# Kernel tuning notes

Measured on AMD Instinct MI355X. Metric: run time of the kernel, lower is better.

The kernel has to match this reference:

```python
import jax, jax.numpy as jnp
import numpy as np

NUM_HEADS = 8
WIN = 4
DIM = 256
EPS = 1e-5


def setup_inputs() -> dict:
    key = jax.random.key(0)
    ks = jax.random.split(key, 5)
    B, C, H, W = 2, DIM, 64, 64
    features = jax.random.normal(ks[0], (B, C, H, W), dtype=jnp.float32)
    # Linear(dim, 3*dim): stored as [C, 3C] so y = x @ qkv_w + qkv_b (matches torch x @ W.T + b)
    qkv_w = jax.random.normal(ks[1], (C, 3 * C), dtype=jnp.float32) * 0.02
    qkv_b = jax.random.normal(ks[2], (3 * C,), dtype=jnp.float32) * 0.02
    out_w = jax.random.normal(ks[3], (C, C), dtype=jnp.float32) * 0.02
    out_b = jax.random.normal(ks[4], (C,), dtype=jnp.float32) * 0.02
    ln_w = jnp.ones((C,), dtype=jnp.float32)
    ln_b = jnp.zeros((C,), dtype=jnp.float32)
    return {"features": features, "qkv_w": qkv_w, "qkv_b": qkv_b,
            "out_w": out_w, "out_b": out_b, "ln_w": ln_w, "ln_b": ln_b}


def reference(features, qkv_w, qkv_b, out_w, out_b, ln_w, ln_b):
    ws = WIN
    B, C, H, W = features.shape
    hc, wc = H // ws, W // ws          # windows per col / row (H,W divisible by ws)
    nW = hc * wc
    Tq = ws * ws
    h, d = NUM_HEADS, C // NUM_HEADS

    # --- query windows: replicate torch unfold(k=ws, s=ws).transpose(1,2).reshape(.., Tq, C)
    # torch unfold layout per window is (c, ki, kj); the reshape reinterprets that flat
    # C*ws*ws vector as [ws*ws, C]. A contiguous reshape reproduces this exactly.
    qwin = features.reshape(B, C, hc, ws, wc, ws).transpose(0, 2, 4, 1, 3, 5)  # [B,hc,wc,C,ws,ws]
    q_tok = qwin.reshape(B, nW, Tq, C)
    # LayerNorm(dim) on query tokens only
    mu = q_tok.mean(-1, keepdims=True)
    var = ((q_tok - mu) ** 2).mean(-1, keepdims=True)
    q_tok = (q_tok - mu) / jnp.sqrt(var + EPS) * ln_w + ln_b

    # --- local KV: unfold(k=2*ws, s=ws) on features padded by ws//2 each side
    lk = 2 * ws
    p = ws // 2
    fp = jnp.pad(features, ((0, 0), (0, 0), (p, p), (p, p)))
    rows = jnp.arange(hc)[:, None] * ws + jnp.arange(lk)[None, :]  # [hc, lk]
    cols = jnp.arange(wc)[:, None] * ws + jnp.arange(lk)[None, :]  # [wc, lk]
    loc = fp[:, :, rows[:, None, :, None], cols[None, :, None, :]]  # [B,C,hc,wc,lk,lk]
    loc = loc.transpose(0, 2, 3, 1, 4, 5).reshape(B, nW, lk * lk, C)  # same layout replica
    Ll = lk * lk

    # --- pooled KV (computed once per batch; the torch expand is a pure broadcast)
    mid = features.reshape(B, C, H // 2, 2, W // 2, 2).mean(axis=(3, 5))
    glb = features.reshape(B, C, H // 4, 4, W // 4, 4).mean(axis=(3, 5))
    mid_tok = mid.reshape(B, C, -1).transpose(0, 2, 1)   # [B, Lm, C]
    glb_tok = glb.reshape(B, C, -1).transpose(0, 2, 1)   # [B, Lg, C]
    Lm = mid_tok.shape[1]

    # --- shared qkv projection; queries use only the Q slice, KV use only K/V slices
    q = (q_tok @ qkv_w + qkv_b)[..., :C]

    def kv(t):
        o = t @ qkv_w + qkv_b
        return o[..., C:2 * C], o[..., 2 * C:]

    kl, vl = kv(loc)
    km, vm = kv(mid_tok)
    kg, vg = kv(glb_tok)

    # heads
    q = q.reshape(B, nW, Tq, h, d).transpose(0, 1, 3, 2, 4)           # [B,nW,h,Tq,d]
    kl = kl.reshape(B, nW, Ll, h, d).transpose(0, 1, 3, 2, 4)
    vl = vl.reshape(B, nW, Ll, h, d).transpose(0, 1, 3, 2, 4)
    km = km.reshape(B, Lm, h, d).transpose(0, 2, 1, 3)                # [B,h,Lm,d]
    vm = vm.reshape(B, Lm, h, d).transpose(0, 2, 1, 3)
    kg = kg.reshape(B, -1, h, d).transpose(0, 2, 1, 3)
    vg = vg.reshape(B, -1, h, d).transpose(0, 2, 1, 3)

    scale = 1.0 / np.sqrt(d).astype(np.float32)
    s_l = jnp.einsum('bwhqd,bwhkd->bwhqk', q, kl)
    s_m = jnp.einsum('bwhqd,bhkd->bwhqk', q, km)
    s_g = jnp.einsum('bwhqd,bhkd->bwhqk', q, kg)
    attn = jax.nn.softmax(jnp.concatenate([s_l, s_m, s_g], axis=-1) * scale, axis=-1)
    a_l = attn[..., :Ll]
    a_m = attn[..., Ll:Ll + Lm]
    a_g = attn[..., Ll + Lm:]
    o = (jnp.einsum('bwhqk,bwhkd->bwhqd', a_l, vl)
         + jnp.einsum('bwhqk,bhkd->bwhqd', a_m, vm)
         + jnp.einsum('bwhqk,bhkd->bwhqd', a_g, vg))

    o = o.transpose(0, 1, 3, 2, 4).reshape(B, nW, Tq, C)
    o = o @ out_w + out_b
    # restore spatial layout: view(B,hc,wc,ws,ws,C).permute(0,5,1,3,2,4).view(B,C,H,W)
    o = o.reshape(B, hc, wc, ws, ws, C).transpose(0, 5, 1, 3, 2, 4).reshape(B, C, H, W)
    return o + features
```

## Files before the change

kernel.cpp:

```cpp
#include <hip/hip_runtime.h>
#include <math.h>

#define HWSZ 4096
#define QSCALE_L2E 0.25501988932587245f

typedef __bf16 bf16x2 __attribute__((ext_vector_type(2)));
typedef __bf16 bf16x4 __attribute__((ext_vector_type(4)));
typedef __bf16 bf16x8 __attribute__((ext_vector_type(8)));
typedef float  f32x4  __attribute__((ext_vector_type(4)));

__global__ __launch_bounds__(256) void fused_pre(
    const float* __restrict__ F, const float* __restrict__ lnw,
    const float* __restrict__ lnb, __bf16* __restrict__ qnb,
    float* __restrict__ mid, float* __restrict__ glb,
    const float* __restrict__ Wqkv, const float* __restrict__ Wout,
    __bf16* __restrict__ WT, __bf16* __restrict__ WoT)
{
  __shared__ float sbuf[64*68];
  int u = blockIdx.x;
  int tid = threadIdx.x;
  if (u < 512) {
    float* sm = sbuf;
    int blk = u;
    int b = blk >> 8, wy = (blk >> 4) & 15, t = blk & 15;
    const float* Fb = F + ((size_t)(b*256 + t*16))*HWSZ + (wy*4)*64;
    int py = tid >> 6, x = tid & 63;
    #pragma unroll
    for (int j = 0; j < 16; ++j)
      sm[j*269 + py*67 + x] = Fb[(size_t)j*HWSZ + py*64 + x];
    __syncthreads();
    int wx = tid >> 4, cl = tid & 15;
    float vals[16], s1 = 0.f, s2 = 0.f;
    #pragma unroll
    for (int p = 0; p < 16; ++p) {
      float v = sm[cl*269 + (p >> 2)*67 + wx*4 + (p & 3)];
      vals[p] = v; s1 += v; s2 += v*v;
    }
    #pragma unroll
    for (int m = 1; m < 16; m <<= 1) { s1 += __shfl_xor(s1, m); s2 += __shfl_xor(s2, m); }
    float mean = s1 * (1.f/256.f);
    float var  = s2 * (1.f/256.f) - mean*mean;
    float rstd = rsqrtf(var + 1e-5f);
    __bf16* outp = qnb + (((size_t)(b*256 + wy*16 + wx))*16 + t)*256 + cl*16;
    bf16x8 o0, o1;
    #pragma unroll
    for (int p = 0; p < 8; ++p) {
      o0[p] = (__bf16)((vals[p]  -mean)*rstd*lnw[cl*16+p]   + lnb[cl*16+p]);
      o1[p] = (__bf16)((vals[p+8]-mean)*rstd*lnw[cl*16+p+8] + lnb[cl*16+p+8]);
    }
    *(bf16x8*)outp = o0;
    *(bf16x8*)(outp+8) = o1;
  } else if (u < 1024) {
    int bc = u - 512;
    int gy = tid >> 4, gx = tid & 15;
    const float* p = F + (size_t)bc*HWSZ + (gy*4)*64 + gx*4;
    float4 r0 = *(const float4*)(p);
    float4 r1 = *(const float4*)(p + 64);
    float4 r2 = *(const float4*)(p + 128);
    float4 r3 = *(const float4*)(p + 192);
    float m00 = 0.25f*(r0.x + r0.y + r1.x + r1.y);
    float m01 = 0.25f*(r0.z + r0.w + r1.z + r1.w);
    float m10 = 0.25f*(r2.x + r2.y + r3.x + r3.y);
    float m11 = 0.25f*(r2.z + r2.w + r3.z + r3.w);
    float* mp = mid + (size_t)bc*1024 + (gy*2)*32 + gx*2;
    *(float2*)mp        = make_float2(m00, m01);
    *(float2*)(mp + 32) = make_float2(m10, m11);
    glb[(size_t)bc*256 + gy*16 + gx] = 0.25f*(m00 + m01 + m10 + m11);
  } else {
    float (*T)[68] = (float(*)[68])sbuf;
    int v = u - 1024;
    int bx = v & 15, k0 = (v >> 4)*64;
    int c4 = (tid & 15)*4, rr = tid >> 4;
    const float* W; __bf16* D; int ncols, n0;
    if (bx < 12) { W = Wqkv; D = WT;  ncols = 768; n0 = bx*64; }
    else         { W = Wout; D = WoT; ncols = 256; n0 = (bx-12)*64; }
    #pragma unroll
    for (int p = 0; p < 4; ++p) {
      int row = p*16 + rr;
      float4 vv = *(const float4*)(W + (size_t)(k0+row)*ncols + n0 + c4);
      T[c4+0][row] = vv.x; T[c4+1][row] = vv.y; T[c4+2][row] = vv.z; T[c4+3][row] = vv.w;
    }
    __syncthreads();
    #pragma unroll
    for (int p = 0; p < 4; ++p) {
      int cc = p*16 + rr;
      bf16x4 o;
      o[0] = (__bf16)T[cc][c4+0]; o[1] = (__bf16)T[cc][c4+1];
      o[2] = (__bf16)T[cc][c4+2]; o[3] = (__bf16)T[cc][c4+3];
      *(bf16x4*)(D + (size_t)(n0+cc)*256 + k0 + c4) = o;
    }
  }
}

__global__ __launch_bounds__(256) void mgt_transpose(
    const float* __restrict__ mid, const float* __restrict__ glb,
    __bf16* __restrict__ mgt)
{
  __shared__ float T[64][68];
  int tt = blockIdx.x;
  int tid = threadIdx.x;
  int c4 = (tid & 15)*4, rr = tid >> 4;
  int b = tt / 20, tq = tt % 20;
  int t0 = tq*64, c0 = blockIdx.y*64;
  const float* src; int stride, toff;
  if (t0 < 1024) { src = mid + ((size_t)(b*256 + c0))*1024; stride = 1024; toff = t0; }
  else           { src = glb + ((size_t)(b*256 + c0))*256;  stride = 256;  toff = t0 - 1024; }
  #pragma unroll
  for (int p = 0; p < 4; ++p) {
    int row = p*16 + rr;
    float4 v = *(const float4*)(src + (size_t)row*stride + toff + c4);
    T[c4+0][row] = v.x; T[c4+1][row] = v.y; T[c4+2][row] = v.z; T[c4+3][row] = v.w;
  }
  __syncthreads();
  #pragma unroll
  for (int p = 0; p < 4; ++p) {
    int t2 = p*16 + rr;
    bf16x4 o;
    o[0] = (__bf16)T[t2][c4+0]; o[1] = (__bf16)T[t2][c4+1];
    o[2] = (__bf16)T[t2][c4+2]; o[3] = (__bf16)T[t2][c4+3];
    *(bf16x4*)(mgt + ((size_t)b*1280 + t0 + t2)*256 + c0 + c4) = o;
  }
}

__global__ __launch_bounds__(256) void fused_gemms(
    const float* __restrict__ F, const __bf16* __restrict__ qnb,
    const __bf16* __restrict__ mgt, const __bf16* __restrict__ WT,
    const float* __restrict__ qkvb,
    __bf16* __restrict__ qbf, __bf16* __restrict__ kloc,
    __bf16* __restrict__ vloct, __bf16* __restrict__ kmg,
    __bf16* __restrict__ vmgt)
{
  __shared__ __bf16 Bs[2][16*264];
  int u = blockIdx.x;
  int tid = threadIdx.x;
  int wv = tid >> 6, lane = tid & 63;
  int col = lane & 15, quad = lane >> 4;
  const f32x4 zero = {0.f,0.f,0.f,0.f};

  if (u < 512) {
    int bw = u;
    int b = bw >> 8, w = bw & 255;
    int wy = w >> 4, wx = w & 15;
    int m0 = wv*16;

    bf16x8 af[8];
    int x0 = wx*4 - 2;
    bool p0ok = (wx > 0), p3ok = (wx < 15);
    const float* Fb = F + ((size_t)(b*256 + 4*(m0+col)))*HWSZ;
    #pragma unroll
    for (int kk = 0; kk < 8; ++kk) {
      int r = kk >> 1;
      int y = wy*4 + (kk & 1)*4 + quad - 2;
      bool yok = ((unsigned)y < 64u);
      const float* row = Fb + (size_t)r*HWSZ + y*64 + x0;
      float2 v0 = make_float2(0.f,0.f), v1 = make_float2(0.f,0.f);
      float2 v2 = make_float2(0.f,0.f), v3 = make_float2(0.f,0.f);
      if (yok) {
        if (p0ok) v0 = *(const float2*)(row);
        v1 = *(const float2*)(row + 2);
        v2 = *(const float2*)(row + 4);
        if (p3ok) v3 = *(const float2*)(row + 6);
      }
      af[kk][0] = (__bf16)v0.x; af[kk][1] = (__bf16)v0.y;
      af[kk][2] = (__bf16)v1.x; af[kk][3] = (__bf16)v1.y;
      af[kk][4] = (__bf16)v2.x; af[kk][5] = (__bf16)v2.y;
      af[kk][6] = (__bf16)v3.x; af[kk][7] = (__bf16)v3.y;
    }

    int brow = tid >> 4, bseg = tid & 15;
    const __bf16* wsrc = WT + ((size_t)(256 + brow))*256 + bseg*16;
    __bf16* bd0 = &Bs[0][0] + brow*264 + bseg*16;
    {
      bf16x8 a0 = *(const bf16x8*)wsrc;
      bf16x8 a1 = *(const bf16x8*)(wsrc + 8);
      *(bf16x8*)bd0 = a0;
      *(bf16x8*)(bd0 + 8) = a1;
    }
    bf16x8 g0 = *(const bf16x8*)(wsrc + (size_t)4096);
    bf16x8 g1 = *(const bf16x8*)(wsrc + (size_t)4096 + 8);
    __syncthreads();

    #pragma unroll 1
    for (int nt = 0; nt < 32; ++nt) {
      if (nt < 31) {
        __bf16* d = &Bs[(nt+1) & 1][0] + brow*264 + bseg*16;
        *(bf16x8*)d = g0;
        *(bf16x8*)(d + 8) = g1;
      }
      if (nt < 30) {
        const __bf16* p = wsrc + (size_t)(nt+2)*4096;
        g0 = *(const bf16x8*)p;
        g1 = *(const bf16x8*)(p + 8);
      }
      int n = nt*16 + col;
      float bias_n = qkvb[256 + n];
      const __bf16* Bb = &Bs[nt & 1][0] + col*264 + quad*8;
      f32x4 acc = zero;
      #pragma unroll
      for (int kk = 0; kk < 8; ++kk) {
        bf16x8 bv = *(const bf16x8*)(Bb + kk*32);
        acc = __builtin_amdgcn_mfma_f32_16x16x32_bf16(af[kk], bv, acc, 0, 0, 0);
      }
      if (nt < 16) {
        #pragma unroll
        for (int r = 0; r < 4; ++r)
          kloc[((size_t)bw*64 + m0 + quad*4 + r)*256 + n] = (__bf16)(acc[r] + bias_n);
      } else {
        bf16x4 o;
        #pragma unroll
        for (int r = 0; r < 4; ++r) o[r] = (__bf16)(acc[r] + bias_n);
        *(bf16x4*)(vloct + ((size_t)bw*256 + (n - 256))*64 + m0 + quad*4) = o;
      }
      __syncthreads();
    }
  } else if (u < 768) {
    int blk = u - 512;
    int tb = blk >> 1, nh = blk & 1;
    int n0 = nh*128;
    int m0 = tb*64 + wv*16;

    bf16x8 bq[8];
    const __bf16* qp = qnb + ((size_t)(m0 + col))*256 + quad*8;
    #pragma unroll
    for (int kk = 0; kk < 8; ++kk) bq[kk] = *(const bf16x8*)(qp + kk*32);

    int brow = tid >> 4, bseg = tid & 15;
    const __bf16* wsrc = WT + ((size_t)(n0 + brow))*256 + bseg*16;
    {
      bf16x8 a0 = *(const bf16x8*)wsrc;
      bf16x8 a1 = *(const bf16x8*)(wsrc + 8);
      __bf16* d = &Bs[0][0] + brow*264 + bseg*16;
      *(bf16x8*)d = a0; *(bf16x8*)(d + 8) = a1;
    }
    bf16x8 g0 = *(const bf16x8*)(wsrc + (size_t)4096);
    bf16x8 g1 = *(const bf16x8*)(wsrc + (size_t)4096 + 8);
    __syncthreads();

    #pragma unroll 1
    for (int s = 0; s < 8; ++s) {
      if (s < 7) {
        __bf16* d = &Bs[(s+1) & 1][0] + brow*264 + bseg*16;
        *(bf16x8*)d = g0; *(bf16x8*)(d + 8) = g1;
      }
      if (s < 6) {
        const __bf16* p = wsrc + (size_t)(s+2)*4096;
        g0 = *(const bf16x8*)p; g1 = *(const bf16x8*)(p + 8);
      }
      const __bf16* Ab = &Bs[s & 1][0] + col*264 + quad*8;
      f32x4 acc = zero;
      #pragma unroll
      for (int kk = 0; kk < 8; ++kk) {
        bf16x8 wf = *(const bf16x8*)(Ab + kk*32);
        acc = __builtin_amdgcn_mfma_f32_16x16x32_bf16(wf, bq[kk], acc, 0, 0, 0);
      }
      int nq4 = n0 + s*16 + quad*4;
      float4 b4 = *(const float4*)(qkvb + nq4);
      float bb[4] = {b4.x, b4.y, b4.z, b4.w};
      bf16x4 o;
      #pragma unroll
      for (int r = 0; r < 4; ++r) o[r] = (__bf16)((acc[r]+bb[r])*QSCALE_L2E);
      *(bf16x4*)(qbf + ((size_t)(m0 + col))*256 + nq4) = o;
      __syncthreads();
    }
  } else {
    int v = u - 768;
    int tb = v % 20, nq = (v / 20) & 3, b = v / 80;
    int m0 = tb*64 + wv*16;
    int n0 = nq*128;

    const __bf16* Ab = mgt + ((size_t)b*1280 + m0 + col)*256 + quad*8;
    bf16x8 af[8];
    #pragma unroll
    for (int kk = 0; kk < 8; ++kk) af[kk] = *(const bf16x8*)(Ab + kk*32);

    int brow = tid >> 4, bseg = tid & 15;
    const __bf16* wsrc = WT + ((size_t)(256 + n0 + brow))*256 + bseg*16;
    {
      bf16x8 a0 = *(const bf16x8*)wsrc;
      bf16x8 a1 = *(const bf16x8*)(wsrc + 8);
      __bf16* d = &Bs[0][0] + brow*264 + bseg*16;
      *(bf16x8*)d = a0; *(bf16x8*)(d + 8) = a1;
    }
    bf16x8 g0 = *(const bf16x8*)(wsrc + (size_t)4096);
    bf16x8 g1 = *(const bf16x8*)(wsrc + (size_t)4096 + 8);
    __syncthreads();

    #pragma unroll 1
    for (int s = 0; s < 8; ++s) {
      if (s < 7) {
        __bf16* d = &Bs[(s+1) & 1][0] + brow*264 + bseg*16;
        *(bf16x8*)d = g0; *(bf16x8*)(d + 8) = g1;
      }
      if (s < 6) {
        const __bf16* p = wsrc + (size_t)(s+2)*4096;
        g0 = *(const bf16x8*)p; g1 = *(const bf16x8*)(p + 8);
      }
      int n = n0 + s*16 + col;
      float bias_n = qkvb[256 + n];
      const __bf16* Bb = &Bs[s & 1][0] + col*264 + quad*8;
      f32x4 acc = zero;
      #pragma unroll
      for (int kk = 0; kk < 8; ++kk) {
        bf16x8 bv = *(const bf16x8*)(Bb + kk*32);
        acc = __builtin_amdgcn_mfma_f32_16x16x32_bf16(af[kk], bv, acc, 0, 0, 0);
      }
      if (n < 256) {
        #pragma unroll
        for (int r = 0; r < 4; ++r)
          kmg[((size_t)b*1280 + m0 + quad*4 + r)*256 + n] = (__bf16)(acc[r] + bias_n);
      } else {
        bf16x4 o;
        #pragma unroll
        for (int r = 0; r < 4; ++r) o[r] = (__bf16)(acc[r] + bias_n);
        *(bf16x4*)(vmgt + ((size_t)b*256 + (n - 256))*1280 + m0 + quad*4) = o;
      }
      __syncthreads();
    }
  }
}

__global__ __launch_bounds__(512) void attn_mfma(
    const __bf16* __restrict__ qbf, const __bf16* __restrict__ kloc,
    const __bf16* __restrict__ vloct, const __bf16* __restrict__ kmg,
    const __bf16* __restrict__ vmgt, __bf16* __restrict__ obf)
{
  __shared__ __bf16 Ks[2][64][40];
  __shared__ __bf16 Vs[2][32][72];
  __shared__ __bf16 Pb[8][2][16][40];
  int blk = blockIdx.x;
  int b = blk >> 8, rr = blk & 255;
  int h = rr >> 5, wg = rr & 31;
  int tid = threadIdx.x, wv = tid >> 6, lane = tid & 63;
  int col = lane & 15, quad = lane >> 4;
  int bw = b*256 + wg*8 + wv;

  bool isK = tid < 256;
  int krow = tid >> 2,        kseg = tid & 3;
  int vrow = (tid - 256) >> 3, vseg = (tid - 256) & 7;
  const __bf16* gbase;
  __bf16 *l0, *l1;
  size_t gslab;
  if (isK) {
    gbase = kmg + ((size_t)(b*1280 + krow))*256 + h*32 + kseg*8;
    gslab = (size_t)64*256;
    l0 = &Ks[0][krow][kseg*8]; l1 = &Ks[1][krow][kseg*8];
  } else {
    gbase = vmgt + ((size_t)(b*256 + h*32 + vrow))*1280 + vseg*8;
    gslab = 64;
    l0 = &Vs[0][vrow][vseg*8]; l1 = &Vs[1][vrow][vseg*8];
  }

  bf16x8 aq = *(const bf16x8*)(qbf + ((size_t)(bw*16 + col))*256 + h*32 + quad*8);
  f32x4 O0 = {0.f,0.f,0.f,0.f}, O1 = {0.f,0.f,0.f,0.f};
  const f32x4 zero = {0.f,0.f,0.f,0.f};
  float ls[4] = {0.f,0.f,0.f,0.f};
  __bf16* PwBase = &Pb[wv][0][0][0];

  bf16x8 sreg = *(const bf16x8*)gbase;

  const __bf16* klocb = kloc  + (size_t)bw*16384 + h*32 + quad*8;
  const __bf16* vlocb = vloct + (size_t)bw*16384 + (size_t)(h*32)*64 + quad*8;
  #pragma unroll
  for (int ch = 0; ch < 2; ++ch) {
    bf16x8 k0 = *(const bf16x8*)(klocb + (size_t)(ch*32 + col)*256);
    bf16x8 k1 = *(const bf16x8*)(klocb + (size_t)(ch*32 + 16 + col)*256);
    bf16x8 v0 = *(const bf16x8*)(vlocb + (size_t)col*64 + ch*32);
    bf16x8 v1 = *(const bf16x8*)(vlocb + (size_t)(16+col)*64 + ch*32);
    f32x4 S0 = __builtin_amdgcn_mfma_f32_16x16x32_bf16(aq, k0, zero, 0, 0, 0);
    f32x4 S1 = __builtin_amdgcn_mfma_f32_16x16x32_bf16(aq, k1, zero, 0, 0, 0);
    __bf16* Pw = PwBase + (ch & 1)*640;
    #pragma unroll
    for (int r = 0; r < 4; ++r) {
      float p0 = __builtin_amdgcn_exp2f(S0[r]);
      float p1 = __builtin_amdgcn_exp2f(S1[r]);
      ls[r] += p0 + p1;
      Pw[(quad*4+r)*40 + col]      = (__bf16)p0;
      Pw[(quad*4+r)*40 + 16 + col] = (__bf16)p1;
    }
    bf16x8 ap = *(const bf16x8*)(Pw + (size_t)col*40 + quad*8);
    O0 = __builtin_amdgcn_mfma_f32_16x16x32_bf16(ap, v0, O0, 0, 0, 0);
    O1 = __builtin_amdgcn_mfma_f32_16x16x32_bf16(ap, v1, O1, 0, 0, 0);
  }

  *(bf16x8*)l0 = sreg;
  sreg = *(const bf16x8*)(gbase + gslab);
  __syncthreads();

  #pragma unroll 1
  for (int s = 0; s < 20; ++s) {
    if (s + 1 < 20) {
      __bf16* ld = (s & 1) ? l0 : l1;
      *(bf16x8*)ld = sreg;
      if (s + 2 < 20) sreg = *(const bf16x8*)(gbase + (size_t)(s+2)*gslab);
    }
    const __bf16* Kb = &Ks[s & 1][0][0];
    const __bf16* Vb = &Vs[s & 1][0][0];
    #pragma unroll
    for (int c = 0; c < 2; ++c) {
      bf16x8 k0 = *(const bf16x8*)(Kb + (c*32 + col)*40 + quad*8);
      bf16x8 k1 = *(const bf16x8*)(Kb + (c*32 + 16 + col)*40 + quad*8);
      bf16x8 v0 = *(const bf16x8*)(Vb + (size_t)col*72 + c*32 + quad*8);
      bf16x8 v1 = *(const bf16x8*)(Vb + (size_t)(16+col)*72 + c*32 + quad*8);
      f32x4 S0 = __builtin_amdgcn_mfma_f32_16x16x32_bf16(aq, k0, zero, 0, 0, 0);
      f32x4 S1 = __builtin_amdgcn_mfma_f32_16x16x32_bf16(aq, k1, zero, 0, 0, 0);
      __bf16* Pw = PwBase + c*640;
      #pragma unroll
      for (int r = 0; r < 4; ++r) {
        float p0 = __builtin_amdgcn_exp2f(S0[r]);
        float p1 = __builtin_amdgcn_exp2f(S1[r]);
        ls[r] += p0 + p1;
        Pw[(quad*4+r)*40 + col]      = (__bf16)p0;
        Pw[(quad*4+r)*40 + 16 + col] = (__bf16)p1;
      }
      bf16x8 ap = *(const bf16x8*)(Pw + (size_t)col*40 + quad*8);
      O0 = __builtin_amdgcn_mfma_f32_16x16x32_bf16(ap, v0, O0, 0, 0, 0);
      O1 = __builtin_amdgcn_mfma_f32_16x16x32_bf16(ap, v1, O1, 0, 0, 0);
    }
    __syncthreads();
  }

  #pragma unroll
  for (int r = 0; r < 4; ++r) {
    #pragma unroll
    for (int m = 1; m < 16; m <<= 1) ls[r] += __shfl_xor(ls[r], m);
  }
  __bf16* op = obf + ((size_t)(bw*16) + quad*4)*256 + h*32 + col;
  #pragma unroll
  for (int r = 0; r < 4; ++r) {
    float inv = 1.f / ls[r];
    op[(size_t)r*256]      = (__bf16)(O0[r]*inv);
    op[(size_t)r*256 + 16] = (__bf16)(O1[r]*inv);
  }
}

__global__ __launch_bounds__(256) void gemm_out_strip(
    const __bf16* __restrict__ obf, const __bf16* __restrict__ WoT,
    const float* __restrict__ outb, const float* __restrict__ Fres,
    float* __restrict__ Out)
{
  __shared__ __bf16 Bs4[4*16*264];
  __shared__ __bf16 strip[64*264];
  int blk = blockIdx.x;
  int b = blk >> 6, wy = (blk >> 2) & 15, cq = blk & 3;
  int c0 = cq*64;
  int tid = threadIdx.x, wv = tid >> 6, lane = tid & 63;
  int col = lane & 15, quad = lane >> 4;
  const f32x4 zero = {0.f,0.f,0.f,0.f};

  {
    int brow = tid >> 4, bseg = tid & 15;
    const __bf16* wsrc = WoT + ((size_t)(c0 + brow))*256 + bseg*16;
    #pragma unroll
    for (int s = 0; s < 4; ++s) {
      bf16x8 a0 = *(const bf16x8*)(wsrc + (size_t)s*4096);
      bf16x8 a1 = *(const bf16x8*)(wsrc + (size_t)s*4096 + 8);
      __bf16* d = Bs4 + s*4224 + brow*264 + bseg*16;
      *(bf16x8*)d = a0; *(bf16x8*)(d + 8) = a1;
    }
  }
  __syncthreads();

  #pragma unroll
  for (int i = 0; i < 4; ++i) {
    int wx = wv*4 + i;
    int win = b*256 + wy*16 + wx;
    bf16x8 ao[8];
    const __bf16* op = obf + ((size_t)win*16 + col)*256 + quad*8;
    #pragma unroll
    for (int kk = 0; kk < 8; ++kk) ao[kk] = *(const bf16x8*)(op + kk*32);
    #pragma unroll
    for (int nt = 0; nt < 4; ++nt) {
      const __bf16* Bb = Bs4 + nt*4224 + col*264 + quad*8;
      f32x4 acc = zero;
      #pragma unroll
      for (int kk = 0; kk < 8; ++kk) {
        bf16x8 wf = *(const bf16x8*)(Bb + kk*32);
        acc = __builtin_amdgcn_mfma_f32_16x16x32_bf16(ao[kk], wf, acc, 0, 0, 0);
      }
      bf16x4 o;
      #pragma unroll
      for (int r = 0; r < 4; ++r) o[r] = (__bf16)acc[r];
      *(bf16x4*)&strip[(nt*16+col)*264 + quad*66 + wx*4] = o;
    }
  }
  __syncthreads();
  #pragma unroll
  for (int j = 0; j < 16; ++j) {
    int f4 = j*256 + tid;
    int xq = f4 & 15, y = (f4 >> 4) & 3, c = f4 >> 6;
    bf16x4 d = *(const bf16x4*)&strip[c*264 + y*66 + xq*4];
    size_t off = ((size_t)(b*256 + c0 + c))*HWSZ + (wy*4 + y)*64 + xq*4;
    float4 r4 = *(const float4*)(Fres + off);
    float bn = outb[c0 + c];
    float4 o;
    o.x = (float)d[0] + bn + r4.x; o.y = (float)d[1] + bn + r4.y;
    o.z = (float)d[2] + bn + r4.z; o.w = (float)d[3] + bn + r4.w;
    *(float4*)(Out + off) = o;
  }
}

extern "C" void kernel_launch(void* const* d_in, const int* in_sizes, int n_in,
                              void* d_out, int out_size, void* d_ws, size_t ws_size,
                              hipStream_t stream) {
  const float* F     = (const float*)d_in[0];
  const float* qkv_w = (const float*)d_in[1];
  const float* qkv_b = (const float*)d_in[2];
  const float* out_w = (const float*)d_in[3];
  const float* out_b = (const float*)d_in[4];
  const float* ln_w  = (const float*)d_in[5];
  const float* ln_b  = (const float*)d_in[6];
  float* out = (float*)d_out;

  __bf16* qnb   = (__bf16*)d_ws;
  __bf16* qbf   = qnb   + 2097152;
  __bf16* obf   = qbf   + 2097152;
  __bf16* kloc  = obf   + 2097152;
  __bf16* vloct = kloc  + 8388608;
  __bf16* kmg   = vloct + 8388608;
  __bf16* vmgt  = kmg   + 655360;
  __bf16* mgt   = vmgt  + 655360;
  __bf16* WT    = mgt   + 655360;
  __bf16* WoT   = WT    + 196608;
  float*  mid   = (float*)(WoT + 65536);
  float*  glb   = mid   + 524288;

  fused_pre<<<1088, 256, 0, stream>>>(F, ln_w, ln_b, qnb, mid, glb,
                                      qkv_w, out_w, WT, WoT);
  mgt_transpose<<<dim3(40, 4), 256, 0, stream>>>(mid, glb, mgt);
  fused_gemms<<<928, 256, 0, stream>>>(F, qnb, mgt, WT, qkv_b,
                                       qbf, kloc, vloct, kmg, vmgt);
  attn_mfma<<<512, 512, 0, stream>>>(qbf, kloc, vloct, kmg, vmgt, obf);
  gemm_out_strip<<<128, 256, 0, stream>>>(obf, WoT, out_b, F, out);
}
```

Before: 153.1 us.

## Keep attention probabilities in registers via transposed MFMA, split out-proj grid

The attention kernel now computes S^T by swapping the MFMA operands, so each lane's exp'd scores already sit in the A-operand layout for the PV MFMA. This removes the per-wave LDS round trip for P, the Pb shared buffer, and most of the row-sum shuffles. To match that layout, V fragments are loaded as two 4-element halves. The output projection kernel also splits each row strip into two x-halves, doubling the grid to 256 blocks for better CU coverage at the cost of reloading the weight tile per block.

```diff
diff --git a/kernel.cpp b/kernel.cpp
--- a/kernel.cpp
+++ b/kernel.cpp
@@ -326,7 +326,6 @@
 {
   __shared__ __bf16 Ks[2][64][40];
   __shared__ __bf16 Vs[2][32][72];
-  __shared__ __bf16 Pb[8][2][16][40];
   int blk = blockIdx.x;
   int b = blk >> 8, rr = blk & 255;
   int h = rr >> 5, wg = rr & 31;
@@ -353,33 +352,34 @@
   bf16x8 aq = *(const bf16x8*)(qbf + ((size_t)(bw*16 + col))*256 + h*32 + quad*8);
   f32x4 O0 = {0.f,0.f,0.f,0.f}, O1 = {0.f,0.f,0.f,0.f};
   const f32x4 zero = {0.f,0.f,0.f,0.f};
-  float ls[4] = {0.f,0.f,0.f,0.f};
-  __bf16* PwBase = &Pb[wv][0][0][0];
+  float ls = 0.f;
 
   bf16x8 sreg = *(const bf16x8*)gbase;
 
   const __bf16* klocb = kloc  + (size_t)bw*16384 + h*32 + quad*8;
-  const __bf16* vlocb = vloct + (size_t)bw*16384 + (size_t)(h*32)*64 + quad*8;
+  const __bf16* vlocb = vloct + (size_t)bw*16384 + (size_t)(h*32)*64;
   #pragma unroll
   for (int ch = 0; ch < 2; ++ch) {
     bf16x8 k0 = *(const bf16x8*)(klocb + (size_t)(ch*32 + col)*256);
     bf16x8 k1 = *(const bf16x8*)(klocb + (size_t)(ch*32 + 16 + col)*256);
-    bf16x8 v0 = *(const bf16x8*)(vlocb + (size_t)col*64 + ch*32);
-    bf16x8 v1 = *(const bf16x8*)(vlocb + (size_t)(16+col)*64 + ch*32);
-    f32x4 S0 = __builtin_amdgcn_mfma_f32_16x16x32_bf16(aq, k0, zero, 0, 0, 0);
-    f32x4 S1 = __builtin_amdgcn_mfma_f32_16x16x32_bf16(aq, k1, zero, 0, 0, 0);
-    __bf16* Pw = PwBase + (ch & 1)*640;
+    bf16x4 va0 = *(const bf16x4*)(vlocb + (size_t)col*64      + ch*32 + quad*4);
+    bf16x4 va1 = *(const bf16x4*)(vlocb + (size_t)col*64      + ch*32 + 16 + quad*4);
+    bf16x4 vb0 = *(const bf16x4*)(vlocb + (size_t)(16+col)*64 + ch*32 + quad*4);
+    bf16x4 vb1 = *(const bf16x4*)(vlocb + (size_t)(16+col)*64 + ch*32 + 16 + quad*4);
+    f32x4 S0 = __builtin_amdgcn_mfma_f32_16x16x32_bf16(k0, aq, zero, 0, 0, 0);
+    f32x4 S1 = __builtin_amdgcn_mfma_f32_16x16x32_bf16(k1, aq, zero, 0, 0, 0);
+    bf16x8 pf;
     #pragma unroll
     for (int r = 0; r < 4; ++r) {
       float p0 = __builtin_amdgcn_exp2f(S0[r]);
       float p1 = __builtin_amdgcn_exp2f(S1[r]);
-      ls[r] += p0 + p1;
-      Pw[(quad*4+r)*40 + col]      = (__bf16)p0;
-      Pw[(quad*4+r)*40 + 16 + col] = (__bf16)p1;
-    }
-    bf16x8 ap = *(const bf16x8*)(Pw + (size_t)col*40 + quad*8);
-    O0 = __builtin_amdgcn_mfma_f32_16x16x32_bf16(ap, v0, O0, 0, 0, 0);
-    O1 = __builtin_amdgcn_mfma_f32_16x16x32_bf16(ap, v1, O1, 0, 0, 0);
+      ls += p0 + p1;
+      pf[r] = (__bf16)p0; pf[4+r] = (__bf16)p1;
+    }
+    bf16x8 v0 = __builtin_shufflevector(va0, va1, 0,1,2,3,4,5,6,7);
+    bf16x8 v1 = __builtin_shufflevector(vb0, vb1, 0,1,2,3,4,5,6,7);
+    O0 = __builtin_amdgcn_mfma_f32_16x16x32_bf16(pf, v0, O0, 0, 0, 0);
+    O1 = __builtin_amdgcn_mfma_f32_16x16x32_bf16(pf, v1, O1, 0, 0, 0);
   }
 
   *(bf16x8*)l0 = sreg;
@@ -399,35 +399,34 @@
     for (int c = 0; c < 2; ++c) {
       bf16x8 k0 = *(const bf16x8*)(Kb + (c*32 + col)*40 + quad*8);
       bf16x8 k1 = *(const bf16x8*)(Kb + (c*32 + 16 + col)*40 + quad*8);
-      bf16x8 v0 = *(const bf16x8*)(Vb + (size_t)col*72 + c*32 + quad*8);
-      bf16x8 v1 = *(const bf16x8*)(Vb + (size_t)(16+col)*72 + c*32 + quad*8);
-      f32x4 S0 = __builtin_amdgcn_mfma_f32_16x16x32_bf16(aq, k0, zero, 0, 0, 0);
-      f32x4 S1 = __builtin_amdgcn_mfma_f32_16x16x32_bf16(aq, k1, zero, 0, 0, 0);
-      __bf16* Pw = PwBase + c*640;
+      bf16x4 va0 = *(const bf16x4*)(Vb + (size_t)col*72      + c*32 + quad*4);
+      bf16x4 va1 = *(const bf16x4*)(Vb + (size_t)col*72      + c*32 + 16 + quad*4);
+      bf16x4 vb0 = *(const bf16x4*)(Vb + (size_t)(16+col)*72 + c*32 + quad*4);
+      bf16x4 vb1 = *(const bf16x4*)(Vb + (size_t)(16+col)*72 + c*32 + 16 + quad*4);
+      f32x4 S0 = __builtin_amdgcn_mfma_f32_16x16x32_bf16(k0, aq, zero, 0, 0, 0);
+      f32x4 S1 = __builtin_amdgcn_mfma_f32_16x16x32_bf16(k1, aq, zero, 0, 0, 0);
+      bf16x8 pf;
       #pragma unroll
       for (int r = 0; r < 4; ++r) {
         float p0 = __builtin_amdgcn_exp2f(S0[r]);
         float p1 = __builtin_amdgcn_exp2f(S1[r]);
-        ls[r] += p0 + p1;
-        Pw[(quad*4+r)*40 + col]      = (__bf16)p0;
-        Pw[(quad*4+r)*40 + 16 + col] = (__bf16)p1;
-      }
-      bf16x8 ap = *(const bf16x8*)(Pw + (size_t)col*40 + quad*8);
-      O0 = __builtin_amdgcn_mfma_f32_16x16x32_bf16(ap, v0, O0, 0, 0, 0);
-      O1 = __builtin_amdgcn_mfma_f32_16x16x32_bf16(ap, v1, O1, 0, 0, 0);
+        ls += p0 + p1;
+        pf[r] = (__bf16)p0; pf[4+r] = (__bf16)p1;
+      }
+      bf16x8 v0 = __builtin_shufflevector(va0, va1, 0,1,2,3,4,5,6,7);
+      bf16x8 v1 = __builtin_shufflevector(vb0, vb1, 0,1,2,3,4,5,6,7);
+      O0 = __builtin_amdgcn_mfma_f32_16x16x32_bf16(pf, v0, O0, 0, 0, 0);
+      O1 = __builtin_amdgcn_mfma_f32_16x16x32_bf16(pf, v1, O1, 0, 0, 0);
     }
     __syncthreads();
   }
 
-  #pragma unroll
-  for (int r = 0; r < 4; ++r) {
-    #pragma unroll
-    for (int m = 1; m < 16; m <<= 1) ls[r] += __shfl_xor(ls[r], m);
-  }
+  ls += __shfl_xor(ls, 16);
+  ls += __shfl_xor(ls, 32);
   __bf16* op = obf + ((size_t)(bw*16) + quad*4)*256 + h*32 + col;
   #pragma unroll
   for (int r = 0; r < 4; ++r) {
-    float inv = 1.f / ls[r];
+    float inv = 1.f / __shfl(ls, quad*4 + r);
     op[(size_t)r*256]      = (__bf16)(O0[r]*inv);
     op[(size_t)r*256 + 16] = (__bf16)(O1[r]*inv);
   }
@@ -441,7 +440,8 @@
   __shared__ __bf16 Bs4[4*16*264];
   __shared__ __bf16 strip[64*264];
   int blk = blockIdx.x;
-  int b = blk >> 6, wy = (blk >> 2) & 15, cq = blk & 3;
+  int b = blk >> 7, rest = blk & 127;
+  int wy = rest >> 3, cq = (rest >> 1) & 3, xh = rest & 1;
   int c0 = cq*64;
   int tid = threadIdx.x, wv = tid >> 6, lane = tid & 63;
   int col = lane & 15, quad = lane >> 4;
@@ -461,8 +461,8 @@
   __syncthreads();
 
   #pragma unroll
-  for (int i = 0; i < 4; ++i) {
-    int wx = wv*4 + i;
+  for (int i = 0; i < 2; ++i) {
+    int wx = xh*8 + wv*2 + i;
     int win = b*256 + wy*16 + wx;
     bf16x8 ao[8];
     const __bf16* op = obf + ((size_t)win*16 + col)*256 + quad*8;
@@ -485,9 +485,9 @@
   }
   __syncthreads();
   #pragma unroll
-  for (int j = 0; j < 16; ++j) {
+  for (int j = 0; j < 8; ++j) {
     int f4 = j*256 + tid;
-    int xq = f4 & 15, y = (f4 >> 4) & 3, c = f4 >> 6;
+    int xq = (f4 & 7) + xh*8, y = (f4 >> 3) & 3, c = f4 >> 5;
     bf16x4 d = *(const bf16x4*)&strip[c*264 + y*66 + xq*4];
     size_t off = ((size_t)(b*256 + c0 + c))*HWSZ + (wy*4 + y)*64 + xq*4;
     float4 r4 = *(const float4*)(Fres + off);
@@ -530,5 +530,5 @@
   fused_gemms<<<928, 256, 0, stream>>>(F, qnb, mgt, WT, qkv_b,
                                        qbf, kloc, vloct, kmg, vmgt);
   attn_mfma<<<512, 512, 0, stream>>>(qbf, kloc, vloct, kmg, vmgt, obf);
-  gemm_out_strip<<<128, 256, 0, stream>>>(obf, WoT, out_b, F, out);
+  gemm_out_strip<<<256, 256, 0, stream>>>(obf, WoT, out_b, F, out);
 }
```

After: 147.0 us. 4.0% less time.
